# Performance work log

Hardware: AMD Instinct MI355X
Metric: run time of the kernel (lower is better)

## Reference

```python
import jax, jax.numpy as jnp
import numpy as np

NUM_GRAPHS = 256


def _gcn_norm(edge_index, num_nodes):
    # Add self-loops and compute symmetric normalization coeffs (PyG gcn_norm).
    loops = jnp.arange(num_nodes, dtype=edge_index.dtype)
    row = jnp.concatenate([edge_index[0], loops])  # source nodes
    col = jnp.concatenate([edge_index[1], loops])  # target nodes
    deg = jax.ops.segment_sum(jnp.ones_like(col, dtype=jnp.float32), col,
                              num_segments=num_nodes)
    dis = jnp.where(deg > 0, jax.lax.rsqrt(jnp.maximum(deg, 1.0)), 0.0)
    norm = dis[row] * dis[col]  # [E + N]
    return row, col, norm


def _gcn_conv(x, row, col, norm, W, b, num_nodes):
    h = x @ W                                        # [N, out] dense transform first
    msg = norm[:, None] * h[row]                     # gather + scale  [E+N, out]
    out = jax.ops.segment_sum(msg, col, num_segments=num_nodes)  # scatter-add
    return out + b


def setup_inputs() -> dict:
    key = jax.random.key(0)
    k = jax.random.split(key, 12)
    N, E, F_IN, H = 100000, 1600000, 64, 64
    x = jax.random.normal(k[0], (N, F_IN), dtype=jnp.float32)
    edge_index = jax.random.randint(k[1], (2, E), 0, N, dtype=jnp.int64)
    batch_index = jnp.sort(jax.random.randint(k[2], (N,), 0, NUM_GRAPHS, dtype=jnp.int64))
    s = 1.0 / np.sqrt(F_IN)
    W1 = jax.random.uniform(k[3], (F_IN, H), minval=-s, maxval=s, dtype=jnp.float32)
    b1 = jnp.zeros((H,), dtype=jnp.float32)
    W2 = jax.random.uniform(k[4], (H, H), minval=-s, maxval=s, dtype=jnp.float32)
    b2 = jnp.zeros((H,), dtype=jnp.float32)
    Wl1 = jax.random.uniform(k[5], (H, H // 2), minval=-s, maxval=s, dtype=jnp.float32)
    bl1 = jax.random.uniform(k[6], (H // 2,), minval=-s, maxval=s, dtype=jnp.float32)
    Wl2 = jax.random.uniform(k[7], (H // 2, 2), minval=-s, maxval=s, dtype=jnp.float32)
    bl2 = jax.random.uniform(k[8], (2,), minval=-s, maxval=s, dtype=jnp.float32)
    return {"x": x, "edge_index": edge_index, "batch_index": batch_index,
            "W1": W1, "b1": b1, "W2": W2, "b2": b2,
            "Wl1": Wl1, "bl1": bl1, "Wl2": Wl2, "bl2": bl2}


def reference(x, edge_index, batch_index, W1, b1, W2, b2, Wl1, bl1, Wl2, bl2):
    N = x.shape[0]
    row, col, norm = _gcn_norm(edge_index, N)
    h = jax.nn.relu(_gcn_conv(x, row, col, norm, W1, b1, N))
    h = jax.nn.relu(_gcn_conv(h, row, col, norm, W2, b2, N))
    # global mean pool over batch_index
    sums = jax.ops.segment_sum(h, batch_index, num_segments=NUM_GRAPHS)
    cnts = jax.ops.segment_sum(jnp.ones((N,), dtype=h.dtype), batch_index,
                               num_segments=NUM_GRAPHS)
    g = sums / jnp.maximum(cnts, 1.0)[:, None]       # [G, H]
    g = jax.nn.relu(g @ Wl1 + bl1)                    # dropout is identity in eval
    logits = g @ Wl2 + bl2
    return jax.nn.log_softmax(logits, axis=1)
```

## Files before the change

### kernel.cpp

```cpp
#include <hip/hip_runtime.h>
#include <hip/hip_fp8.h>
#include <cstdint>
#include <cstddef>


#define HF 64
#define BSH 8
#define BSZ 256
#define PCHUNK 4096
#define PADB 6144
#define CNTCLAMP (PADB - 4 * BSZ)
#define POISON 0xAAAAAAAAu
#define NG 256

typedef unsigned u32;

__device__ __forceinline__ unsigned short f2bf(float x) {
    unsigned u = __float_as_uint(x);
    unsigned r = (u + 0x7fffu + ((u >> 16) & 1u)) >> 16;
    return (unsigned short)r;
}
__device__ __forceinline__ float bfl(u32 w) { return __uint_as_float(w << 16); }
__device__ __forceinline__ float bfh(u32 w) { return __uint_as_float(w & 0xffff0000u); }

__device__ __forceinline__ u32 pack_fp8x4(float a, float b, float c, float d) {
#if __has_builtin(__builtin_amdgcn_cvt_pk_fp8_f32)
    int v = 0;
    v = __builtin_amdgcn_cvt_pk_fp8_f32(a, b, v, false);
    v = __builtin_amdgcn_cvt_pk_fp8_f32(c, d, v, true);
    return (u32)v;
#else
    __hip_fp8_e4m3 fa(a), fb(b), fc(c), fd(d);
    return (u32)fa.__x | ((u32)fb.__x << 8) | ((u32)fc.__x << 16) | ((u32)fd.__x << 24);
#endif
}
__device__ __forceinline__ void acc_fp8x4(float4& acc, u32 w) {
#if __has_builtin(__builtin_amdgcn_cvt_pk_f32_fp8)
    typedef float v2f __attribute__((ext_vector_type(2)));
    v2f lo = __builtin_amdgcn_cvt_pk_f32_fp8((int)w, false);
    v2f hi = __builtin_amdgcn_cvt_pk_f32_fp8((int)w, true);
    acc.x += lo[0]; acc.y += lo[1]; acc.z += hi[0]; acc.w += hi[1];
#else
    __hip_fp8_e4m3 a, b, c, d;
    a.__x = (unsigned char)(w);       b.__x = (unsigned char)(w >> 8);
    c.__x = (unsigned char)(w >> 16); d.__x = (unsigned char)(w >> 24);
    acc.x += (float)a; acc.y += (float)b; acc.z += (float)c; acc.w += (float)d;
#endif
}

__global__ __launch_bounds__(256) void k_part(const int* __restrict__ rows,
                                              const int* __restrict__ cols,
                                              u32* __restrict__ gcurb,
                                              u32* __restrict__ part, int E) {
    __shared__ u32 hist[512];
    __shared__ u32 off[512];
    __shared__ u32 obase[512];
    __shared__ u32 cur[512];
    __shared__ u32 sc[256];
    __shared__ u32 stage[PCHUNK];
    __shared__ unsigned short sbk[PCHUNK];
    const int tid = threadIdx.x;
    const int e0  = blockIdx.x * PCHUNK;
    u32 er[16], ec[16];

    hist[tid] = 0; hist[tid + 256] = 0;
    __syncthreads();
#pragma unroll
    for (int j = 0; j < 16; ++j) {
        int e = e0 + j * 256 + tid;
        if (e < E) {
            ec[j] = (u32)cols[e];
            er[j] = (u32)rows[e];
            atomicAdd(&hist[ec[j] >> BSH], 1u);
        } else ec[j] = 0xFFFFFFFFu;
    }
    __syncthreads();
    u32 c0 = hist[2 * tid], c1 = hist[2 * tid + 1];
    u32 s = c0 + c1;
    sc[tid] = s;
    __syncthreads();
    for (int o = 1; o < 256; o <<= 1) {
        u32 t = (tid >= o) ? sc[tid - o] : 0u;
        __syncthreads();
        sc[tid] += t;
        __syncthreads();
    }
    u32 ex = sc[tid] - s;
    off[2 * tid] = ex;          cur[2 * tid] = ex;
    off[2 * tid + 1] = ex + c0; cur[2 * tid + 1] = ex + c0;
    obase[2 * tid]     = c0 ? (atomicAdd(&gcurb[2 * tid], c0) - POISON) : 0u;
    obase[2 * tid + 1] = c1 ? (atomicAdd(&gcurb[2 * tid + 1], c1) - POISON) : 0u;
    __syncthreads();
#pragma unroll
    for (int j = 0; j < 16; ++j) {
        if (ec[j] != 0xFFFFFFFFu) {
            u32 bk  = ec[j] >> BSH;
            u32 pos = atomicAdd(&cur[bk], 1u);
            stage[pos] = ((ec[j] & (BSZ - 1)) << 17) | er[j];
            sbk[pos]   = (unsigned short)bk;
        }
    }
    __syncthreads();
    const int total = (e0 + PCHUNK <= E) ? PCHUNK : (E - e0);
    for (int i = tid; i < total; i += 256) {
        u32 bk = sbk[i];
        u32 pb = obase[bk] + ((u32)i - off[bk]);
        if (pb < PADB)
            part[(size_t)bk * PADB + pb] = stage[i];
    }
}

__global__ __launch_bounds__(256) void k_place2(const u32* __restrict__ gcurb,
                                                const u32* __restrict__ part,
                                                const float* __restrict__ x,
                                                u32* __restrict__ rowptr,
                                                float* __restrict__ dis,
                                                u32* __restrict__ s08,
                                                u32* __restrict__ h18,
                                                int* __restrict__ eidx,
                                                float* __restrict__ gm,
                                                int N, float S0) {
    __shared__ u32 cnt_[256];
    __shared__ u32 off_[257];
    __shared__ u32 sc[256];
    __shared__ u32 cur[256];
    __shared__ u32 outb[PADB];
    const int tid = threadIdx.x;
    const int b   = blockIdx.x;
    const int n0  = b << BSH;
    const u32 base = (u32)b * PADB;
    u32 cntB = gcurb[b] - POISON; if (cntB > CNTCLAMP) cntB = CNTCLAMP;

    if (b == 0 && tid < 16) {
        s08[(size_t)N * 16 + tid] = 0u;
        h18[(size_t)N * 16 + tid] = 0u;
    }
    if (b == 0) {
        for (int i = tid; i < NG * HF; i += 256) gm[i] = 0.f;
    }

    cnt_[tid] = 0;
    __syncthreads();
    for (u32 i = tid; i < cntB; i += 256)
        atomicAdd(&cnt_[part[base + i] >> 17], 1u);
    __syncthreads();
    u32 v  = cnt_[tid];
    bool live = (n0 + tid) < N;
    u32 vs = v + 1u;
    u32 p  = live ? ((vs + 3u) & ~3u) : 0u;
    sc[tid] = p;
    __syncthreads();
    for (int o = 1; o < 256; o <<= 1) {
        u32 t = (tid >= o) ? sc[tid - o] : 0u;
        __syncthreads();
        sc[tid] += t;
        __syncthreads();
    }
    u32 ex = sc[tid] - p;
    off_[tid] = ex; cur[tid] = ex;
    if (tid == 255) off_[256] = sc[255];
    __syncthreads();
    const u32 cntP = off_[256];
    if (live) {
        u32 dg = vs; if (dg > 1023u) dg = 1023u;
        rowptr[n0 + tid] = (base + ex) | (dg << 22);
        dis[n0 + tid]    = rsqrtf(1.0f + (float)v);
    }
    {
        int nmax = min(256, N - n0);
        for (int idx = tid; idx < nmax * 16; idx += 256) {
            int nl = idx >> 4, f4 = idx & 15;
            float d  = S0 * rsqrtf(1.0f + (float)cnt_[nl]);
            float4 xv = ((const float4*)(x + (size_t)(n0 + nl) * HF))[f4];
            s08[(size_t)(n0 + nl) * 16 + f4] =
                pack_fp8x4(d * xv.x, d * xv.y, d * xv.z, d * xv.w);
        }
    }
    for (u32 i = tid; i < cntP; i += 256) outb[i] = (u32)N;
    __syncthreads();
    for (u32 i = tid; i < cntB; i += 256) {
        u32 pv  = part[base + i];
        u32 pos = atomicAdd(&cur[pv >> 17], 1u);
        outb[pos] = pv & 0x1FFFFu;
    }
    __syncthreads();
    if (live) outb[cur[tid]] = (u32)tid;
    __syncthreads();
    for (u32 i = tid; i < cntP; i += 256)
        eidx[base + i] = (int)outb[i];
}

template <int OUTFP8>
__global__ __launch_bounds__(512, 8) void k_gtrans(const u32* __restrict__ rowptr,
                                                   const int* __restrict__ eidx,
                                                   const u32* __restrict__ hs8,
                                                   const float* __restrict__ W,
                                                   const float* __restrict__ dis,
                                                   const float* __restrict__ bias,
                                                   void* __restrict__ OUTp, int N,
                                                   float invS, float outS) {
    __shared__ float ws[64 * 64];
    __shared__ u32 xs2[128 * 34];
    const int tid  = threadIdx.x;
    const int row0 = blockIdx.x * 128;

#pragma unroll
    for (int i = 0; i < 2; ++i) {
        int idx4 = i * 512 + tid;
        *(float4*)&ws[idx4 * 4] = ((const float4*)W)[idx4];
    }

    const int qq = tid >> 4;
    const int f4 = tid & 15;
#pragma unroll 1
    for (int j = 0; j < 4; ++j) {
        const int nl = qq * 4 + j;
        const int n  = row0 + nl;
        float4 acc = float4{0.f, 0.f, 0.f, 0.f};
        if (n < N) {
            u32 rp    = rowptr[n];
            u32 start = rp & 0x3FFFFFu;
            int ngr   = (int)(((rp >> 22) + 3u) >> 2);
            const uint4* eb = (const uint4*)(eidx + start);
            int g = 0;
            for (; g + 1 < ngr; g += 2) {
                uint4 ea  = eb[g];
                uint4 eb2 = eb[g + 1];
                u32 wa0 = hs8[(size_t)ea.x * 16 + f4];
                u32 wa1 = hs8[(size_t)ea.y * 16 + f4];
                u32 wa2 = hs8[(size_t)ea.z * 16 + f4];
                u32 wa3 = hs8[(size_t)ea.w * 16 + f4];
                u32 wb0 = hs8[(size_t)eb2.x * 16 + f4];
                u32 wb1 = hs8[(size_t)eb2.y * 16 + f4];
                u32 wb2 = hs8[(size_t)eb2.z * 16 + f4];
                u32 wb3 = hs8[(size_t)eb2.w * 16 + f4];
                acc_fp8x4(acc, wa0); acc_fp8x4(acc, wa1);
                acc_fp8x4(acc, wa2); acc_fp8x4(acc, wa3);
                acc_fp8x4(acc, wb0); acc_fp8x4(acc, wb1);
                acc_fp8x4(acc, wb2); acc_fp8x4(acc, wb3);
            }
            if (g < ngr) {
                uint4 ea = eb[g];
                u32 w0 = hs8[(size_t)ea.x * 16 + f4];
                u32 w1 = hs8[(size_t)ea.y * 16 + f4];
                u32 w2 = hs8[(size_t)ea.z * 16 + f4];
                u32 w3 = hs8[(size_t)ea.w * 16 + f4];
                acc_fp8x4(acc, w0); acc_fp8x4(acc, w1);
                acc_fp8x4(acc, w2); acc_fp8x4(acc, w3);
            }
        }
        u32 lo = (u32)f2bf(acc.x) | ((u32)f2bf(acc.y) << 16);
        u32 hi = (u32)f2bf(acc.z) | ((u32)f2bf(acc.w) << 16);
        xs2[nl * 34 + f4 * 2]     = lo;
        xs2[nl * 34 + f4 * 2 + 1] = hi;
    }
    __syncthreads();

    const int rg = tid >> 4;
    const int cg = tid & 15;
    float4 a0 = float4{0.f, 0.f, 0.f, 0.f};
    float4 a1 = a0, a2 = a0, a3 = a0;

#pragma unroll 4
    for (int k2 = 0; k2 < 32; ++k2) {
        float4 wv0 = *(float4*)&ws[(2 * k2)     * 64 + cg * 4];
        float4 wv1 = *(float4*)&ws[(2 * k2 + 1) * 64 + cg * 4];
        u32 p0 = xs2[(rg * 4 + 0) * 34 + k2];
        u32 p1 = xs2[(rg * 4 + 1) * 34 + k2];
        u32 p2 = xs2[(rg * 4 + 2) * 34 + k2];
        u32 p3 = xs2[(rg * 4 + 3) * 34 + k2];
        float x0e = bfl(p0), x0o = bfh(p0);
        float x1e = bfl(p1), x1o = bfh(p1);
        float x2e = bfl(p2), x2o = bfh(p2);
        float x3e = bfl(p3), x3o = bfh(p3);
        a0.x += x0e * wv0.x; a0.y += x0e * wv0.y; a0.z += x0e * wv0.z; a0.w += x0e * wv0.w;
        a1.x += x1e * wv0.x; a1.y += x1e * wv0.y; a1.z += x1e * wv0.z; a1.w += x1e * wv0.w;
        a2.x += x2e * wv0.x; a2.y += x2e * wv0.y; a2.z += x2e * wv0.z; a2.w += x2e * wv0.w;
        a3.x += x3e * wv0.x; a3.y += x3e * wv0.y; a3.z += x3e * wv0.z; a3.w += x3e * wv0.w;
        a0.x += x0o * wv1.x; a0.y += x0o * wv1.y; a0.z += x0o * wv1.z; a0.w += x0o * wv1.w;
        a1.x += x1o * wv1.x; a1.y += x1o * wv1.y; a1.z += x1o * wv1.z; a1.w += x1o * wv1.w;
        a2.x += x2o * wv1.x; a2.y += x2o * wv1.y; a2.z += x2o * wv1.z; a2.w += x2o * wv1.w;
        a3.x += x3o * wv1.x; a3.y += x3o * wv1.y; a3.z += x3o * wv1.z; a3.w += x3o * wv1.w;
    }

    float4 bv = ((const float4*)bias)[cg];
    float4 accs[4] = {a0, a1, a2, a3};
#pragma unroll
    for (int j = 0; j < 4; ++j) {
        int row = row0 + rg * 4 + j;
        if (row < N) {
            float d  = dis[row];
            float dd = d * invS;
            float4 a = accs[j];
            a.x = fmaxf(dd * a.x + bv.x, 0.f);
            a.y = fmaxf(dd * a.y + bv.y, 0.f);
            a.z = fmaxf(dd * a.z + bv.z, 0.f);
            a.w = fmaxf(dd * a.w + bv.w, 0.f);
            if (OUTFP8) {
                float so = d * outS;
                ((u32*)OUTp)[(size_t)row * 16 + cg] =
                    pack_fp8x4(so * a.x, so * a.y, so * a.z, so * a.w);
            } else {
                ushort4 pk;
                pk.x = f2bf(a.x); pk.y = f2bf(a.y);
                pk.z = f2bf(a.z); pk.w = f2bf(a.w);
                *(ushort4*)&((unsigned short*)OUTp)[(size_t)row * HF + cg * 4] = pk;
            }
        }
    }
}

__device__ __forceinline__ int lower_bound(const int* __restrict__ a, int n, int key) {
    int lo = 0, hi = n;
    while (lo < hi) { int mid = (lo + hi) >> 1; if (a[mid] < key) lo = mid + 1; else hi = mid; }
    return lo;
}

__global__ __launch_bounds__(256) void k_pool(const u32* __restrict__ h2,
                                              const int* __restrict__ batch,
                                              float* __restrict__ gm, int N) {
    __shared__ float red[4][64];
    const int g    = blockIdx.x >> 2;
    const int sl   = blockIdx.x & 3;
    const int lane = threadIdx.x & 63;
    const int w    = threadIdx.x >> 6;
    int s = lower_bound(batch, N, g);
    int e = lower_bound(batch, N, g + 1);
    int len = e - s;
    int q0 = s + ((len * sl) >> 2);
    int q1 = s + ((len * (sl + 1)) >> 2);
    float acc = 0.f;
    for (int n = q0 + w; n < q1; n += 4) {
        u32 wv = h2[(size_t)n * 32 + (lane >> 1)];
        acc += (lane & 1) ? bfh(wv) : bfl(wv);
    }
    red[w][lane] = acc;
    __syncthreads();
    if (w == 0) {
        float t = red[0][lane] + red[1][lane] + red[2][lane] + red[3][lane];
        atomicAdd(&gm[g * HF + lane], t);
    }
}

__global__ __launch_bounds__(64) void k_head(const float* __restrict__ gm,
                                             const int* __restrict__ batch,
                                             const float* __restrict__ Wl1,
                                             const float* __restrict__ bl1,
                                             const float* __restrict__ Wl2,
                                             const float* __restrict__ bl2,
                                             float* __restrict__ out, int N) {
    __shared__ float gml[64];
    const int g    = blockIdx.x;
    const int lane = threadIdx.x;
    int s = lower_bound(batch, N, g);
    int e = lower_bound(batch, N, g + 1);
    gml[lane] = gm[g * HF + lane] / fmaxf((float)(e - s), 1.0f);
    __syncthreads();
    if (lane < 32) {
        float a = bl1[lane];
#pragma unroll
        for (int k = 0; k < 64; ++k) a += gml[k] * Wl1[k * 32 + lane];
        a = fmaxf(a, 0.f);
        float l0 = a * Wl2[2 * lane];
        float l1 = a * Wl2[2 * lane + 1];
#pragma unroll
        for (int o = 1; o < 32; o <<= 1) {
            l0 += __shfl_xor(l0, o);
            l1 += __shfl_xor(l1, o);
        }
        if (lane == 0) {
            l0 += bl2[0]; l1 += bl2[1];
            float m   = fmaxf(l0, l1);
            float lse = m + logf(expf(l0 - m) + expf(l1 - m));
            out[2 * g]     = l0 - lse;
            out[2 * g + 1] = l1 - lse;
        }
    }
}

extern "C" void kernel_launch(void* const* d_in, const int* in_sizes, int n_in,
                              void* d_out, int out_size, void* d_ws, size_t ws_size,
                              hipStream_t stream) {
    const float* x   = (const float*)d_in[0];
    const int*   ei  = (const int*)d_in[1];
    const int*   bi  = (const int*)d_in[2];
    const float* W1  = (const float*)d_in[3];
    const float* b1  = (const float*)d_in[4];
    const float* W2  = (const float*)d_in[5];
    const float* b2  = (const float*)d_in[6];
    const float* Wl1 = (const float*)d_in[7];
    const float* bl1 = (const float*)d_in[8];
    const float* Wl2 = (const float*)d_in[9];
    const float* bl2 = (const float*)d_in[10];
    float* out = (float*)d_out;

    const int N = in_sizes[0] / HF;
    const int E = in_sizes[1] / 2;
    const int* rows = ei;
    const int* cols = ei + E;
    const int NB = (N + BSZ - 1) / BSZ;
    const size_t EP = (size_t)NB * PADB;

    const float S0 = 4.0f, S1 = 16.0f;

    float* ws = (float*)d_ws;
    size_t o = 0;
    float* dis    = ws + o; o += ((size_t)N + 63) / 64 * 64;
    u32*   A8     = (u32*)(ws + o); o += (size_t)(N + 1) * 16;
    u32*   B8     = (u32*)(ws + o); o += (size_t)(N + 1) * 16;
    unsigned short* Cbf = (unsigned short*)(ws + o); o += (size_t)N * 32;
    u32*   rowptr = (u32*)(ws + o); o += ((size_t)N + 63) / 64 * 64;
    u32*   part   = (u32*)(ws + o); o += EP;
    int*   eidx   = (int*)(ws + o); o += EP;
    u32*   gcurb  = (u32*)(ws + o); o += 512;
    float* gm     = ws + o; o += (size_t)NG * HF;

    const int tb = (N + 127) / 128;

    k_part<<<(E + PCHUNK - 1) / PCHUNK, 256, 0, stream>>>(rows, cols, gcurb, part, E);
    k_place2<<<NB, 256, 0, stream>>>(gcurb, part, x, rowptr, dis, A8, B8, eidx, gm, N, S0);

    k_gtrans<1><<<tb, 512, 0, stream>>>(rowptr, eidx, A8, W1, dis, b1, (void*)B8,
                                        N, 1.0f / S0, S1);
    k_gtrans<0><<<tb, 512, 0, stream>>>(rowptr, eidx, B8, W2, dis, b2, (void*)Cbf,
                                        N, 1.0f / S1, 0.f);

    k_pool<<<NG * 4, 256, 0, stream>>>((const u32*)Cbf, bi, gm, N);
    k_head<<<NG, 64, 0, stream>>>(gm, bi, Wl1, bl1, Wl2, bl2, out, N);
}
```

Measured before the change: 236.4 us.

## Fuse global mean pooling into second GCN layer and use nontemporal loads

The second graph-transform kernel now accumulates its ReLU outputs into per-block shared-memory pool slots, keyed by batch id, and atomically adds them to the global graph sums. This removes the bf16 intermediate write, the separate pooling kernel and its binary searches. It assumes each 128-row tile spans at most two graphs, which sorted batches with large graphs satisfy. Streaming index and input loads are also switched to nontemporal loads, and rowptr is fetched as a 4-wide vector.

New measurement: 267.1 us. 13.0% more time.

```diff
diff --git a/kernel.cpp b/kernel.cpp
--- a/kernel.cpp
+++ b/kernel.cpp
@@ -14,6 +14,8 @@
 #define NG 256
 
 typedef unsigned u32;
+typedef unsigned v4u __attribute__((ext_vector_type(4)));
+typedef float    v4f __attribute__((ext_vector_type(4)));
 
 __device__ __forceinline__ unsigned short f2bf(float x) {
     unsigned u = __float_as_uint(x);
@@ -69,8 +71,8 @@
     for (int j = 0; j < 16; ++j) {
         int e = e0 + j * 256 + tid;
         if (e < E) {
-            ec[j] = (u32)cols[e];
-            er[j] = (u32)rows[e];
+            ec[j] = (u32)__builtin_nontemporal_load(cols + e);
+            er[j] = (u32)__builtin_nontemporal_load(rows + e);
             atomicAdd(&hist[ec[j] >> BSH], 1u);
         } else ec[j] = 0xFFFFFFFFu;
     }
@@ -142,7 +144,7 @@
     cnt_[tid] = 0;
     __syncthreads();
     for (u32 i = tid; i < cntB; i += 256)
-        atomicAdd(&cnt_[part[base + i] >> 17], 1u);
+        atomicAdd(&cnt_[__builtin_nontemporal_load(part + base + i) >> 17], 1u);
     __syncthreads();
     u32 v  = cnt_[tid];
     bool live = (n0 + tid) < N;
@@ -171,9 +173,10 @@
         for (int idx = tid; idx < nmax * 16; idx += 256) {
             int nl = idx >> 4, f4 = idx & 15;
             float d  = S0 * rsqrtf(1.0f + (float)cnt_[nl]);
-            float4 xv = ((const float4*)(x + (size_t)(n0 + nl) * HF))[f4];
+            v4f xv = __builtin_nontemporal_load(
+                (const v4f*)(x + (size_t)(n0 + nl) * HF) + f4);
             s08[(size_t)(n0 + nl) * 16 + f4] =
-                pack_fp8x4(d * xv.x, d * xv.y, d * xv.z, d * xv.w);
+                pack_fp8x4(d * xv[0], d * xv[1], d * xv[2], d * xv[3]);
         }
     }
     for (u32 i = tid; i < cntP; i += 256) outb[i] = (u32)N;
@@ -197,12 +200,24 @@
                                                    const float* __restrict__ W,
                                                    const float* __restrict__ dis,
                                                    const float* __restrict__ bias,
-                                                   void* __restrict__ OUTp, int N,
-                                                   float invS, float outS) {
+                                                   u32* __restrict__ OUT8,
+                                                   float* __restrict__ gm,
+                                                   const int* __restrict__ batch,
+                                                   int N, float invS, float outS) {
     __shared__ float ws[64 * 64];
     __shared__ u32 xs2[128 * 34];
+    __shared__ int   sbg[128];
+    __shared__ float pool[128];
     const int tid  = threadIdx.x;
     const int row0 = blockIdx.x * 128;
+
+    if constexpr (!OUTFP8) {
+        if (tid < 128) {
+            int r = row0 + tid;
+            sbg[tid]  = (r < N) ? batch[r] : -1;
+            pool[tid] = 0.f;
+        }
+    }
 
 #pragma unroll
     for (int i = 0; i < 2; ++i) {
@@ -212,39 +227,41 @@
 
     const int qq = tid >> 4;
     const int f4 = tid & 15;
+    const int nb0 = row0 + qq * 4;
+    v4u rp4 = *(const v4u*)(rowptr + nb0);
 #pragma unroll 1
     for (int j = 0; j < 4; ++j) {
         const int nl = qq * 4 + j;
         const int n  = row0 + nl;
         float4 acc = float4{0.f, 0.f, 0.f, 0.f};
         if (n < N) {
-            u32 rp    = rowptr[n];
+            u32 rp    = rp4[j];
             u32 start = rp & 0x3FFFFFu;
             int ngr   = (int)(((rp >> 22) + 3u) >> 2);
-            const uint4* eb = (const uint4*)(eidx + start);
+            const v4u* eb = (const v4u*)(eidx + start);
             int g = 0;
             for (; g + 1 < ngr; g += 2) {
-                uint4 ea  = eb[g];
-                uint4 eb2 = eb[g + 1];
-                u32 wa0 = hs8[(size_t)ea.x * 16 + f4];
-                u32 wa1 = hs8[(size_t)ea.y * 16 + f4];
-                u32 wa2 = hs8[(size_t)ea.z * 16 + f4];
-                u32 wa3 = hs8[(size_t)ea.w * 16 + f4];
-                u32 wb0 = hs8[(size_t)eb2.x * 16 + f4];
-                u32 wb1 = hs8[(size_t)eb2.y * 16 + f4];
-                u32 wb2 = hs8[(size_t)eb2.z * 16 + f4];
-                u32 wb3 = hs8[(size_t)eb2.w * 16 + f4];
+                v4u ea  = __builtin_nontemporal_load(eb + g);
+                v4u eb2 = __builtin_nontemporal_load(eb + g + 1);
+                u32 wa0 = hs8[(size_t)ea[0] * 16 + f4];
+                u32 wa1 = hs8[(size_t)ea[1] * 16 + f4];
+                u32 wa2 = hs8[(size_t)ea[2] * 16 + f4];
+                u32 wa3 = hs8[(size_t)ea[3] * 16 + f4];
+                u32 wb0 = hs8[(size_t)eb2[0] * 16 + f4];
+                u32 wb1 = hs8[(size_t)eb2[1] * 16 + f4];
+                u32 wb2 = hs8[(size_t)eb2[2] * 16 + f4];
+                u32 wb3 = hs8[(size_t)eb2[3] * 16 + f4];
                 acc_fp8x4(acc, wa0); acc_fp8x4(acc, wa1);
                 acc_fp8x4(acc, wa2); acc_fp8x4(acc, wa3);
                 acc_fp8x4(acc, wb0); acc_fp8x4(acc, wb1);
                 acc_fp8x4(acc, wb2); acc_fp8x4(acc, wb3);
             }
             if (g < ngr) {
-                uint4 ea = eb[g];
-                u32 w0 = hs8[(size_t)ea.x * 16 + f4];
-                u32 w1 = hs8[(size_t)ea.y * 16 + f4];
-                u32 w2 = hs8[(size_t)ea.z * 16 + f4];
-                u32 w3 = hs8[(size_t)ea.w * 16 + f4];
+                v4u ea = __builtin_nontemporal_load(eb + g);
+                u32 w0 = hs8[(size_t)ea[0] * 16 + f4];
+                u32 w1 = hs8[(size_t)ea[1] * 16 + f4];
+                u32 w2 = hs8[(size_t)ea[2] * 16 + f4];
+                u32 w3 = hs8[(size_t)ea[3] * 16 + f4];
                 acc_fp8x4(acc, w0); acc_fp8x4(acc, w1);
                 acc_fp8x4(acc, w2); acc_fp8x4(acc, w3);
             }
@@ -285,6 +302,7 @@
 
     float4 bv = ((const float4*)bias)[cg];
     float4 accs[4] = {a0, a1, a2, a3};
+    const int g0s = OUTFP8 ? 0 : sbg[0];
 #pragma unroll
     for (int j = 0; j < 4; ++j) {
         int row = row0 + rg * 4 + j;
@@ -296,16 +314,27 @@
             a.y = fmaxf(dd * a.y + bv.y, 0.f);
             a.z = fmaxf(dd * a.z + bv.z, 0.f);
             a.w = fmaxf(dd * a.w + bv.w, 0.f);
-            if (OUTFP8) {
+            if constexpr (OUTFP8) {
                 float so = d * outS;
-                ((u32*)OUTp)[(size_t)row * 16 + cg] =
+                OUT8[(size_t)row * 16 + cg] =
                     pack_fp8x4(so * a.x, so * a.y, so * a.z, so * a.w);
             } else {
-                ushort4 pk;
-                pk.x = f2bf(a.x); pk.y = f2bf(a.y);
-                pk.z = f2bf(a.z); pk.w = f2bf(a.w);
-                *(ushort4*)&((unsigned short*)OUTp)[(size_t)row * HF + cg * 4] = pk;
+                int slot = (sbg[rg * 4 + j] != g0s) ? 64 : 0;
+                atomicAdd(&pool[slot + cg * 4 + 0], a.x);
+                atomicAdd(&pool[slot + cg * 4 + 1], a.y);
+                atomicAdd(&pool[slot + cg * 4 + 2], a.z);
+                atomicAdd(&pool[slot + cg * 4 + 3], a.w);
             }
+        }
+    }
+    if constexpr (!OUTFP8) {
+        __syncthreads();
+        int lastv = N - 1 - row0; if (lastv > 127) lastv = 127;
+        const int g1s = sbg[lastv];
+        if (tid < 64) {
+            atomicAdd(&gm[g0s * HF + tid], pool[tid]);
+        } else if (tid < 128 && g1s != g0s) {
+            atomicAdd(&gm[g1s * HF + (tid - 64)], pool[tid]);
         }
     }
 }
@@ -314,32 +343,6 @@
     int lo = 0, hi = n;
     while (lo < hi) { int mid = (lo + hi) >> 1; if (a[mid] < key) lo = mid + 1; else hi = mid; }
     return lo;
-}
-
-__global__ __launch_bounds__(256) void k_pool(const u32* __restrict__ h2,
-                                              const int* __restrict__ batch,
-                                              float* __restrict__ gm, int N) {
-    __shared__ float red[4][64];
-    const int g    = blockIdx.x >> 2;
-    const int sl   = blockIdx.x & 3;
-    const int lane = threadIdx.x & 63;
-    const int w    = threadIdx.x >> 6;
-    int s = lower_bound(batch, N, g);
-    int e = lower_bound(batch, N, g + 1);
-    int len = e - s;
-    int q0 = s + ((len * sl) >> 2);
-    int q1 = s + ((len * (sl + 1)) >> 2);
-    float acc = 0.f;
-    for (int n = q0 + w; n < q1; n += 4) {
-        u32 wv = h2[(size_t)n * 32 + (lane >> 1)];
-        acc += (lane & 1) ? bfh(wv) : bfl(wv);
-    }
-    red[w][lane] = acc;
-    __syncthreads();
-    if (w == 0) {
-        float t = red[0][lane] + red[1][lane] + red[2][lane] + red[3][lane];
-        atomicAdd(&gm[g * HF + lane], t);
-    }
 }
 
 __global__ __launch_bounds__(64) void k_head(const float* __restrict__ gm,
@@ -408,7 +411,6 @@
     float* dis    = ws + o; o += ((size_t)N + 63) / 64 * 64;
     u32*   A8     = (u32*)(ws + o); o += (size_t)(N + 1) * 16;
     u32*   B8     = (u32*)(ws + o); o += (size_t)(N + 1) * 16;
-    unsigned short* Cbf = (unsigned short*)(ws + o); o += (size_t)N * 32;
     u32*   rowptr = (u32*)(ws + o); o += ((size_t)N + 63) / 64 * 64;
     u32*   part   = (u32*)(ws + o); o += EP;
     int*   eidx   = (int*)(ws + o); o += EP;
@@ -420,11 +422,10 @@
     k_part<<<(E + PCHUNK - 1) / PCHUNK, 256, 0, stream>>>(rows, cols, gcurb, part, E);
     k_place2<<<NB, 256, 0, stream>>>(gcurb, part, x, rowptr, dis, A8, B8, eidx, gm, N, S0);
 
-    k_gtrans<1><<<tb, 512, 0, stream>>>(rowptr, eidx, A8, W1, dis, b1, (void*)B8,
+    k_gtrans<1><<<tb, 512, 0, stream>>>(rowptr, eidx, A8, W1, dis, b1, B8, gm, bi,
                                         N, 1.0f / S0, S1);
-    k_gtrans<0><<<tb, 512, 0, stream>>>(rowptr, eidx, B8, W2, dis, b2, (void*)Cbf,
+    k_gtrans<0><<<tb, 512, 0, stream>>>(rowptr, eidx, B8, W2, dis, b2, nullptr, gm, bi,
                                         N, 1.0f / S1, 0.f);
 
-    k_pool<<<NG * 4, 256, 0, stream>>>((const u32*)Cbf, bi, gm, N);
     k_head<<<NG, 64, 0, stream>>>(gm, bi, Wl1, bl1, Wl2, bl2, out, N);
 }
```
